# Performance work log

Hardware: AMD Instinct MI355X
Metric: run time of the kernel (lower is better)

The kernel has to match this reference:

```python
import jax, jax.numpy as jnp
import numpy as np

EPS = 1e-08
SIGMA = 0.1
B = 1.0


def setup_inputs() -> dict:
    key = jax.random.key(0)
    k1, k2 = jax.random.split(key)
    N, C, H, W = 4, 256, 64, 64
    featureT = jax.random.normal(k1, (N, C, H, W), dtype=jnp.float32)
    featureI = jax.random.normal(k2, (N, C, H, W), dtype=jnp.float32)
    return {"featureT": featureT, "featureI": featureI}


def reference(featureT, featureI):
    N, C, H, W = featureT.shape
    # center both by target mean over (batch, spatial)
    meanT = featureT.mean(axis=(0, 2, 3), keepdims=True)
    fI = featureI - meanT
    fT = featureT - meanT
    # channel-wise L2 normalize
    fI = fI / (jnp.linalg.norm(fI, axis=1, keepdims=True) + EPS)
    fT = fT / (jnp.linalg.norm(fT, axis=1, keepdims=True) + EPS)
    # 1x1-patch conv2d == contraction over channels: sim[n, p, h, w]
    # where p indexes the flattened H*W spatial positions of the target.
    fT_flat = fT.reshape(N, C, H * W)  # [N, C, P]
    sim = jnp.einsum('nchw,ncp->nphw', fI, fT_flat)  # [N, P, H, W]
    raw_dist = (1.0 - sim) / 2.0
    # relative distances: divide by min over patch axis
    div = jnp.min(raw_dist, axis=1, keepdims=True)
    relative_dist = raw_dist / (div + EPS)
    # contextual similarity: exp-weight + sum-normalize over patch axis
    Wt = jnp.exp((B - relative_dist) / (SIGMA + EPS))
    W_sum = Wt.sum(axis=1, keepdims=True)
    CX = Wt / (W_sum + EPS)
    # max over spatial dims of featureI, mean over patches, -log, mean over batch
    CX = CX.max(axis=(2, 3))           # [N, P]
    CX = CX.mean(axis=1)               # [N]
    CX_loss = -jnp.log(CX + EPS)
    return jnp.mean(CX_loss)
```

## Files before the change

### kernel.cpp

```cpp
#include <hip/hip_runtime.h>
#include <cmath>


#define NB 4
#define CC 256
#define HW 4096
#define NQ 8

static constexpr float kEPS = 1e-8f;
static constexpr float kSIG = 0.1f + 1e-8f;

typedef __attribute__((ext_vector_type(8)))  short short8;
typedef __attribute__((ext_vector_type(16))) float f32x16;

enum {
  OFF_MEAN = 0,
  OFF_CMAX = 256,
  OFF_WSUM = OFF_CMAX + NQ*NB*HW,
  OFF_MAXV = OFF_WSUM + NQ*NB*HW,
  OFF_GT   = OFF_MAXV + NQ*NB*HW,
  OFF_GI   = OFF_GT + NB*HW*CC/2,
  WS_FLOATS_FULL = OFF_GI + NB*HW*CC/2
};

__device__ __forceinline__ ushort cvt_bf16(float x) {
  unsigned u = __float_as_uint(x);
  unsigned r = (u + 0x7fffu + ((u >> 16) & 1u)) >> 16;
  return (ushort)r;
}

__device__ __forceinline__ float blockSum256(float v) {
  __shared__ float sh[4];
  const int lane = threadIdx.x & 63, wv = threadIdx.x >> 6;
  #pragma unroll
  for (int o = 32; o > 0; o >>= 1) v += __shfl_down(v, o, 64);
  __syncthreads();
  if (lane == 0) sh[wv] = v;
  __syncthreads();
  return sh[0] + sh[1] + sh[2] + sh[3];
}

__global__ __launch_bounds__(256) void k_mean8(const float* __restrict__ fT,
                                               float* __restrict__ ws) {
  const int c = blockIdx.x, t = threadIdx.x;
  float s = 0.f;
  for (int n = 0; n < NB; ++n) {
    const float* p = fT + (size_t)(n*CC + c)*HW;
    #pragma unroll
    for (int k = 0; k < 16; ++k) s += p[k*256 + t];
  }
  const float tot = blockSum256(s);
  if (t == 0) ws[OFF_MEAN + c] = tot * (1.0f/16384.0f);
}

__global__ __launch_bounds__(256) void k_prep8(const float* __restrict__ fT,
                                               const float* __restrict__ fI,
                                               float* __restrict__ ws) {
  __shared__ float stage[32][257];
  __shared__ float prt[8][32];
  __shared__ float sinv[32];
  const int t = threadIdx.x, l = t & 63;
  int bid = blockIdx.x;
  const int tensor = (bid >= 512); bid &= 511;
  const int n   = bid >> 7;
  const int r32 = bid & 127;
  const int p0  = r32 * 32;

  const float* __restrict__ src = tensor ? fI : fT;
  ushort* __restrict__ dst = (ushort*)(ws + (tensor ? OFF_GI : OFF_GT));
  const float* __restrict__ mean = ws + OFF_MEAN;

  const int pl = t & 31, cg = t >> 5;
  float acc = 0.f;
  #pragma unroll
  for (int i = 0; i < 32; ++i) {
    const int c = cg*32 + i;
    const float v = src[((size_t)(n*CC + c))*HW + p0 + pl] - mean[c];
    stage[pl][c] = v;
    acc += v*v;
  }
  prt[cg][pl] = acc;
  __syncthreads();
  if (t < 32) {
    float s = 0.f;
    #pragma unroll
    for (int g = 0; g < 8; ++g) s += prt[g][t];
    sinv[t] = 1.0f/(sqrtf(s) + kEPS);
  }
  __syncthreads();

  const int w = t >> 6, lhi = l >> 5, m = l & 31;
  const float iv = sinv[m];
  #pragma unroll
  for (int i = 0; i < 4; ++i) {
    const int kc = w*4 + i;
    const int cb = kc*16 + lhi*8;
    short8 o;
    #pragma unroll
    for (int j = 0; j < 8; ++j)
      ((ushort*)&o)[j] = cvt_bf16(stage[m][cb + j] * iv);
    *(short8*)(dst + (((size_t)(n*128 + r32)*16 + kc) << 9) + l*8) = o;
  }
}

__global__ __launch_bounds__(256, 4) void k_sweep_mfma8(
    const ushort* __restrict__ gA, const ushort* __restrict__ gB,
    float* __restrict__ ws, const int mode)
{
  __shared__ ushort Ab[2][8192];
  __shared__ float red2[128];
  __shared__ float gall[512], ball[512];

  const int t = threadIdx.x;
  const int w = t >> 6, l = t & 63;
  const int ln31 = l & 31, lhi = l >> 5;

  const int b = blockIdx.x;
  const int h = b & 7, sid = b >> 3;
  const int n = sid >> 5;
  const int col0 = (sid & 31) * 128;
  const int loop0 = h * 512;

  const ushort* __restrict__ gAn = gA + (size_t)(n*128 + h*16)*8192;

  short8 pf[4];
  #pragma unroll
  for (int i = 0; i < 4; ++i)
    pf[i] = *(const short8*)(gAn + (size_t)(i*256 + t)*8);
  #pragma unroll
  for (int i = 0; i < 4; ++i)
    *(short8*)&Ab[0][(i*256 + t)*8] = pf[i];
  #pragma unroll
  for (int i = 0; i < 4; ++i)
    pf[i] = *(const short8*)(gAn + 8192 + (size_t)(i*256 + t)*8);

  const int RB = (col0 >> 5) + w;
  short8 breg[16];
  #pragma unroll
  for (int kc = 0; kc < 16; ++kc)
    breg[kc] = *(const short8*)(gB +
        (((size_t)(n*128 + RB)*16 + kc) << 9) + l*8);

  float aq = 0.f, bq = 0.f;
  if (mode == 1) {
    const int q = col0 + w*32 + ln31;
    float cm = -3.0e38f;
    #pragma unroll
    for (int hh = 0; hh < NQ; ++hh)
      cm = fmaxf(cm, ws[OFF_CMAX + hh*(NB*HW) + n*HW + q]);
    const float div   = 0.5f*(1.0f - cm);
    const float inv2d = 1.0f/(2.0f*(div + kEPS));
    bq = inv2d / kSIG;
    aq = (1.0f - inv2d) / kSIG;
  }
  if (mode == 2) {
    #pragma unroll
    for (int i = 0; i < 2; ++i) {
      const int r = i*256 + t;
      const int q = loop0 + r;
      float cm = -3.0e38f, sw = 0.f;
      #pragma unroll
      for (int hh = 0; hh < NQ; ++hh) {
        cm = fmaxf(cm, ws[OFF_CMAX + hh*(NB*HW) + n*HW + q]);
        sw += ws[OFF_WSUM + hh*(NB*HW) + n*HW + q];
      }
      const float div   = 0.5f*(1.0f - cm);
      const float inv2d = 1.0f/(2.0f*(div + kEPS));
      const float beta  = inv2d / kSIG;
      const float alpha = (1.0f - inv2d) / kSIG;
      ball[r] = beta;
      gall[r] = alpha - logf(sw + kEPS);
    }
  }

  float runl = (mode == 1) ? 0.0f : -3.0e38f;

  for (int iter = 0; iter < 16; ++iter) {
    const int p = iter & 1;
    __syncthreads();
    if (iter + 1 < 16) {
      #pragma unroll
      for (int i = 0; i < 4; ++i)
        *(short8*)&Ab[p^1][(i*256 + t)*8] = pf[i];
      if (iter + 2 < 16) {
        const ushort* __restrict__ src = gAn + (size_t)(iter + 2)*8192;
        #pragma unroll
        for (int i = 0; i < 4; ++i)
          pf[i] = *(const short8*)(src + (size_t)(i*256 + t)*8);
      }
    }

    f32x16 acc;
    #pragma unroll
    for (int e = 0; e < 16; ++e) acc[e] = 0.f;

    #pragma unroll
    for (int kc = 0; kc < 16; ++kc) {
      const short8 a0 = *(const short8*)&Ab[p][kc*512 + l*8];
      acc = __builtin_amdgcn_mfma_f32_32x32x16_bf16(a0, breg[kc], acc, 0, 0, 0);
    }

    if (mode == 0) {
      float m = runl;
      #pragma unroll
      for (int r = 0; r < 16; ++r) m = fmaxf(m, acc[r]);
      runl = m;
    } else if (mode == 1) {
      float s = 0.f;
      #pragma unroll
      for (int r = 0; r < 16; ++r) s += __expf(fmaf(bq, acc[r], aq));
      runl += s;
    } else {
      const int tb = iter*32 + 4*lhi;
      float m = runl;
      #pragma unroll
      for (int rg = 0; rg < 4; ++rg) {
        const int rb = tb + 8*rg;
        const float4 g4 = *(const float4*)&gall[rb];
        const float4 b4 = *(const float4*)&ball[rb];
        m = fmaxf(m, fmaf(b4.x, acc[rg*4+0], g4.x));
        m = fmaxf(m, fmaf(b4.y, acc[rg*4+1], g4.y));
        m = fmaxf(m, fmaf(b4.z, acc[rg*4+2], g4.z));
        m = fmaxf(m, fmaf(b4.w, acc[rg*4+3], g4.w));
      }
      runl = m;
    }
  }

  {
    const float o = __shfl_xor(runl, 32, 64);
    runl = (mode == 1) ? (runl + o) : fmaxf(runl, o);
  }
  if (l < 32) red2[w*32 + ln31] = runl;
  __syncthreads();
  if (t < 128) {
    const int base = (mode == 0) ? OFF_CMAX : ((mode == 1) ? OFF_WSUM : OFF_MAXV);
    ws[base + h*(NB*HW) + n*HW + col0 + t] = red2[t];
  }
}

__global__ __launch_bounds__(256) void k_final8(const float* __restrict__ ws,
                                                float* __restrict__ out) {
  const int t = threadIdx.x;
  float loss = 0.f;
  for (int n = 0; n < NB; ++n) {
    float s = 0.f;
    for (int k = 0; k < 16; ++k) {
      const int idx = n*HW + k*256 + t;
      float mv = ws[OFF_MAXV + idx];
      #pragma unroll
      for (int h = 1; h < NQ; ++h) mv = fmaxf(mv, ws[OFF_MAXV + h*(NB*HW) + idx]);
      s += __expf(mv);
    }
    const float tot = blockSum256(s);
    loss += -logf(tot*(1.0f/4096.0f) + kEPS);
  }
  if (t == 0) out[0] = loss*0.25f;
}

extern "C" void kernel_launch(void* const* d_in, const int* in_sizes, int n_in,
                              void* d_out, int out_size, void* d_ws, size_t ws_size,
                              hipStream_t stream) {
  const float* fT = (const float*)d_in[0];
  const float* fI = (const float*)d_in[1];
  float* out = (float*)d_out;
  float* ws  = (float*)d_ws;

  const size_t need_full = (size_t)WS_FLOATS_FULL * sizeof(float);
  if (ws_size < need_full) return;

  const ushort* GT = (const ushort*)(ws + OFF_GT);
  const ushort* GI = (const ushort*)(ws + OFF_GI);
  k_mean8      <<<256,  256, 0, stream>>>(fT, ws);
  k_prep8      <<<1024, 256, 0, stream>>>(fT, fI, ws);
  k_sweep_mfma8<<<1024, 256, 0, stream>>>(GT, GI, ws, 0);
  k_sweep_mfma8<<<1024, 256, 0, stream>>>(GT, GI, ws, 1);
  k_sweep_mfma8<<<1024, 256, 0, stream>>>(GI, GT, ws, 2);
  k_final8     <<<1,    256, 0, stream>>>(ws, out);
}
```

Baseline: 213.9 us.

## Materialize the similarity matrix once in bf16 instead of recomputing the GEMM three times

Replaces the three full MFMA sweeps (column max, exp-sum, final max) with one GEMM that writes the full per-batch similarity matrix to workspace as bf16. It also records column maxima. Two bandwidth-bound passes then read that matrix: the first computes partial exp-sums, and the second computes row maxima using precomputed per-column alpha/beta. This removes two redundant GEMMs but adds hundreds of MB of HBM write and read traffic, strided scalar stores from the GEMM, and bf16 rounding of similarities before the exp.

Result: faster. 205.1 us (-4.1%).

```diff
diff --git a/kernel.cpp b/kernel.cpp
--- a/kernel.cpp
+++ b/kernel.cpp
@@ -5,7 +5,8 @@
 #define NB 4
 #define CC 256
 #define HW 4096
-#define NQ 8
+#define NQ0 8
+#define NP1 32
 
 static constexpr float kEPS = 1e-8f;
 static constexpr float kSIG = 0.1f + 1e-8f;
@@ -16,11 +17,13 @@
 enum {
   OFF_MEAN = 0,
   OFF_CMAX = 256,
-  OFF_WSUM = OFF_CMAX + NQ*NB*HW,
-  OFF_MAXV = OFF_WSUM + NQ*NB*HW,
-  OFF_GT   = OFF_MAXV + NQ*NB*HW,
+  OFF_WSUM = OFF_CMAX + NQ0*NB*HW,
+  OFF_MAXV = OFF_WSUM + NP1*NB*HW,
+  OFF_GB   = OFF_MAXV + NB*HW,
+  OFF_GT   = OFF_GB + 2*NB*HW,
   OFF_GI   = OFF_GT + NB*HW*CC/2,
-  WS_FLOATS_FULL = OFF_GI + NB*HW*CC/2
+  OFF_S    = OFF_GI + NB*HW*CC/2,
+  WS_FLOATS_FULL = OFF_S + NB*HW*HW/2
 };
 
 __device__ __forceinline__ ushort cvt_bf16(float x) {
@@ -28,6 +31,9 @@
   unsigned r = (u + 0x7fffu + ((u >> 16) & 1u)) >> 16;
   return (ushort)r;
 }
+__device__ __forceinline__ float bf2f(ushort u) {
+  return __uint_as_float((unsigned)u << 16);
+}
 
 __device__ __forceinline__ float blockSum256(float v) {
   __shared__ float sh[4];
@@ -40,7 +46,7 @@
   return sh[0] + sh[1] + sh[2] + sh[3];
 }
 
-__global__ __launch_bounds__(256) void k_mean8(const float* __restrict__ fT,
+__global__ __launch_bounds__(256) void k_mean9(const float* __restrict__ fT,
                                                float* __restrict__ ws) {
   const int c = blockIdx.x, t = threadIdx.x;
   float s = 0.f;
@@ -53,7 +59,7 @@
   if (t == 0) ws[OFF_MEAN + c] = tot * (1.0f/16384.0f);
 }
 
-__global__ __launch_bounds__(256) void k_prep8(const float* __restrict__ fT,
+__global__ __launch_bounds__(256) void k_prep9(const float* __restrict__ fT,
                                                const float* __restrict__ fI,
                                                float* __restrict__ ws) {
   __shared__ float stage[32][257];
@@ -103,13 +109,12 @@
   }
 }
 
-__global__ __launch_bounds__(256, 4) void k_sweep_mfma8(
+__global__ __launch_bounds__(256, 4) void k_gemm9(
     const ushort* __restrict__ gA, const ushort* __restrict__ gB,
-    float* __restrict__ ws, const int mode)
+    float* __restrict__ ws)
 {
   __shared__ ushort Ab[2][8192];
   __shared__ float red2[128];
-  __shared__ float gall[512], ball[512];
 
   const int t = threadIdx.x;
   const int w = t >> 6, l = t & 63;
@@ -119,7 +124,6 @@
   const int h = b & 7, sid = b >> 3;
   const int n = sid >> 5;
   const int col0 = (sid & 31) * 128;
-  const int loop0 = h * 512;
 
   const ushort* __restrict__ gAn = gA + (size_t)(n*128 + h*16)*8192;
 
@@ -141,39 +145,10 @@
     breg[kc] = *(const short8*)(gB +
         (((size_t)(n*128 + RB)*16 + kc) << 9) + l*8);
 
-  float aq = 0.f, bq = 0.f;
-  if (mode == 1) {
-    const int q = col0 + w*32 + ln31;
-    float cm = -3.0e38f;
-    #pragma unroll
-    for (int hh = 0; hh < NQ; ++hh)
-      cm = fmaxf(cm, ws[OFF_CMAX + hh*(NB*HW) + n*HW + q]);
-    const float div   = 0.5f*(1.0f - cm);
-    const float inv2d = 1.0f/(2.0f*(div + kEPS));
-    bq = inv2d / kSIG;
-    aq = (1.0f - inv2d) / kSIG;
-  }
-  if (mode == 2) {
-    #pragma unroll
-    for (int i = 0; i < 2; ++i) {
-      const int r = i*256 + t;
-      const int q = loop0 + r;
-      float cm = -3.0e38f, sw = 0.f;
-      #pragma unroll
-      for (int hh = 0; hh < NQ; ++hh) {
-        cm = fmaxf(cm, ws[OFF_CMAX + hh*(NB*HW) + n*HW + q]);
-        sw += ws[OFF_WSUM + hh*(NB*HW) + n*HW + q];
-      }
-      const float div   = 0.5f*(1.0f - cm);
-      const float inv2d = 1.0f/(2.0f*(div + kEPS));
-      const float beta  = inv2d / kSIG;
-      const float alpha = (1.0f - inv2d) / kSIG;
-      ball[r] = beta;
-      gall[r] = alpha - logf(sw + kEPS);
-    }
-  }
-
-  float runl = (mode == 1) ? 0.0f : -3.0e38f;
+  const int qc = col0 + w*32 + ln31;
+  ushort* __restrict__ Sq = (ushort*)(ws + OFF_S) + (size_t)n*HW*HW + qc;
+
+  float runl = -3.0e38f;
 
   for (int iter = 0; iter < 16; ++iter) {
     const int p = iter & 1;
@@ -193,65 +168,127 @@
     f32x16 acc;
     #pragma unroll
     for (int e = 0; e < 16; ++e) acc[e] = 0.f;
-
     #pragma unroll
     for (int kc = 0; kc < 16; ++kc) {
       const short8 a0 = *(const short8*)&Ab[p][kc*512 + l*8];
       acc = __builtin_amdgcn_mfma_f32_32x32x16_bf16(a0, breg[kc], acc, 0, 0, 0);
     }
 
-    if (mode == 0) {
-      float m = runl;
-      #pragma unroll
-      for (int r = 0; r < 16; ++r) m = fmaxf(m, acc[r]);
-      runl = m;
-    } else if (mode == 1) {
-      float s = 0.f;
-      #pragma unroll
-      for (int r = 0; r < 16; ++r) s += __expf(fmaf(bq, acc[r], aq));
-      runl += s;
-    } else {
-      const int tb = iter*32 + 4*lhi;
-      float m = runl;
-      #pragma unroll
-      for (int rg = 0; rg < 4; ++rg) {
-        const int rb = tb + 8*rg;
-        const float4 g4 = *(const float4*)&gall[rb];
-        const float4 b4 = *(const float4*)&ball[rb];
-        m = fmaxf(m, fmaf(b4.x, acc[rg*4+0], g4.x));
-        m = fmaxf(m, fmaf(b4.y, acc[rg*4+1], g4.y));
-        m = fmaxf(m, fmaf(b4.z, acc[rg*4+2], g4.z));
-        m = fmaxf(m, fmaf(b4.w, acc[rg*4+3], g4.w));
-      }
-      runl = m;
+    const int pb = h*512 + iter*32 + 4*lhi;
+    #pragma unroll
+    for (int r = 0; r < 16; ++r) {
+      const int prow = pb + (r & 3) + 8*(r >> 2);
+      const ushort u = cvt_bf16(acc[r]);
+      Sq[(size_t)prow * HW] = u;
+      runl = fmaxf(runl, bf2f(u));
     }
   }
 
   {
     const float o = __shfl_xor(runl, 32, 64);
-    runl = (mode == 1) ? (runl + o) : fmaxf(runl, o);
+    runl = fmaxf(runl, o);
   }
   if (l < 32) red2[w*32 + ln31] = runl;
   __syncthreads();
-  if (t < 128) {
-    const int base = (mode == 0) ? OFF_CMAX : ((mode == 1) ? OFF_WSUM : OFF_MAXV);
-    ws[base + h*(NB*HW) + n*HW + col0 + t] = red2[t];
-  }
-}
-
-__global__ __launch_bounds__(256) void k_final8(const float* __restrict__ ws,
+  if (t < 128)
+    ws[OFF_CMAX + h*(NB*HW) + n*HW + col0 + t] = red2[t];
+}
+
+__global__ __launch_bounds__(256) void k_pass1(float* __restrict__ ws) {
+  const int t = threadIdx.x;
+  const int b = blockIdx.x;
+  const int pc = b & 31, rest = b >> 5;
+  const int n = rest >> 3, qblk = rest & 7;
+  const int q = qblk*512 + 2*t;
+
+  float a0, b0, a1, b1;
+  {
+    float cm0 = -3.0e38f, cm1 = -3.0e38f;
+    #pragma unroll
+    for (int hh = 0; hh < NQ0; ++hh) {
+      cm0 = fmaxf(cm0, ws[OFF_CMAX + hh*(NB*HW) + n*HW + q]);
+      cm1 = fmaxf(cm1, ws[OFF_CMAX + hh*(NB*HW) + n*HW + q + 1]);
+    }
+    const float i0 = 1.0f/(2.0f*(0.5f*(1.0f - cm0) + kEPS));
+    const float i1 = 1.0f/(2.0f*(0.5f*(1.0f - cm1) + kEPS));
+    b0 = i0 / kSIG; a0 = (1.0f - i0) / kSIG;
+    b1 = i1 / kSIG; a1 = (1.0f - i1) / kSIG;
+  }
+
+  const ushort* __restrict__ S =
+      (const ushort*)(ws + OFF_S) + (size_t)n*HW*HW + q;
+  float acc0 = 0.f, acc1 = 0.f;
+  const int p0 = pc*128;
+  #pragma unroll 8
+  for (int i = 0; i < 128; ++i) {
+    const ushort2 u = *(const ushort2*)(S + (size_t)(p0 + i)*HW);
+    acc0 += __expf(fmaf(b0, bf2f(u.x), a0));
+    acc1 += __expf(fmaf(b1, bf2f(u.y), a1));
+  }
+  float2 o; o.x = acc0; o.y = acc1;
+  *(float2*)&ws[OFF_WSUM + pc*(NB*HW) + n*HW + q] = o;
+}
+
+__global__ __launch_bounds__(256) void k_gb9(float* __restrict__ ws) {
+  const int idx = blockIdx.x*256 + threadIdx.x;
+  float cm = -3.0e38f;
+  #pragma unroll
+  for (int hh = 0; hh < NQ0; ++hh)
+    cm = fmaxf(cm, ws[OFF_CMAX + hh*(NB*HW) + idx]);
+  const float inv2d = 1.0f/(2.0f*(0.5f*(1.0f - cm) + kEPS));
+  const float beta  = inv2d / kSIG;
+  const float alpha = (1.0f - inv2d) / kSIG;
+  float sw = 0.f;
+  #pragma unroll
+  for (int pc = 0; pc < NP1; ++pc)
+    sw += ws[OFF_WSUM + pc*(NB*HW) + idx];
+  ws[OFF_GB + idx]         = alpha - logf(sw + kEPS);
+  ws[OFF_GB + NB*HW + idx] = beta;
+}
+
+__global__ __launch_bounds__(256) void k_pass2(float* __restrict__ ws) {
+  __shared__ float gq[4096], bq[4096];
+  const int t = threadIdx.x, w = t >> 6, l = t & 63;
+  const int b = blockIdx.x;
+  const int n = b >> 8, pg = b & 255;
+
+  const float* __restrict__ G  = ws + OFF_GB + n*HW;
+  const float* __restrict__ Bq = ws + OFF_GB + NB*HW + n*HW;
+  #pragma unroll
+  for (int i = 0; i < 4; ++i) {
+    *(float4*)&gq[(i*256 + t)*4] = *(const float4*)&G [(i*256 + t)*4];
+    *(float4*)&bq[(i*256 + t)*4] = *(const float4*)&Bq[(i*256 + t)*4];
+  }
+  __syncthreads();
+
+  const ushort* __restrict__ S =
+      (const ushort*)(ws + OFF_S) + (size_t)n*HW*HW;
+  #pragma unroll
+  for (int r = 0; r < 4; ++r) {
+    const int p = pg*16 + w*4 + r;
+    const ushort* __restrict__ row = S + (size_t)p*HW;
+    float m = -3.0e38f;
+    #pragma unroll 4
+    for (int it = 0; it < 32; ++it) {
+      const int q = it*128 + 2*l;
+      const ushort2 u = *(const ushort2*)(row + q);
+      m = fmaxf(m, fmaf(bq[q],     bf2f(u.x), gq[q]));
+      m = fmaxf(m, fmaf(bq[q + 1], bf2f(u.y), gq[q + 1]));
+    }
+    #pragma unroll
+    for (int o = 32; o > 0; o >>= 1) m = fmaxf(m, __shfl_xor(m, o, 64));
+    if (l == 0) ws[OFF_MAXV + n*HW + p] = m;
+  }
+}
+
+__global__ __launch_bounds__(256) void k_final9(const float* __restrict__ ws,
                                                 float* __restrict__ out) {
   const int t = threadIdx.x;
   float loss = 0.f;
   for (int n = 0; n < NB; ++n) {
     float s = 0.f;
-    for (int k = 0; k < 16; ++k) {
-      const int idx = n*HW + k*256 + t;
-      float mv = ws[OFF_MAXV + idx];
-      #pragma unroll
-      for (int h = 1; h < NQ; ++h) mv = fmaxf(mv, ws[OFF_MAXV + h*(NB*HW) + idx]);
-      s += __expf(mv);
-    }
+    for (int k = 0; k < 16; ++k)
+      s += __expf(ws[OFF_MAXV + n*HW + k*256 + t]);
     const float tot = blockSum256(s);
     loss += -logf(tot*(1.0f/4096.0f) + kEPS);
   }
@@ -271,10 +308,11 @@
 
   const ushort* GT = (const ushort*)(ws + OFF_GT);
   const ushort* GI = (const ushort*)(ws + OFF_GI);
-  k_mean8      <<<256,  256, 0, stream>>>(fT, ws);
-  k_prep8      <<<1024, 256, 0, stream>>>(fT, fI, ws);
-  k_sweep_mfma8<<<1024, 256, 0, stream>>>(GT, GI, ws, 0);
-  k_sweep_mfma8<<<1024, 256, 0, stream>>>(GT, GI, ws, 1);
-  k_sweep_mfma8<<<1024, 256, 0, stream>>>(GI, GT, ws, 2);
-  k_final8     <<<1,    256, 0, stream>>>(ws, out);
-}
+  k_mean9 <<<256,  256, 0, stream>>>(fT, ws);
+  k_prep9 <<<1024, 256, 0, stream>>>(fT, fI, ws);
+  k_gemm9 <<<1024, 256, 0, stream>>>(GT, GI, ws);
+  k_pass1 <<<1024, 256, 0, stream>>>(ws);
+  k_gb9   <<<64,   256, 0, stream>>>(ws);
+  k_pass2 <<<1024, 256, 0, stream>>>(ws);
+  k_final9<<<1,    256, 0, stream>>>(ws, out);
+}
```
